# Kernel tuning notes

Hardware: AMD Instinct MI355X
Metric: run time of the kernel (lower is better)

Reference implementation:

```python
import jax, jax.numpy as jnp
import numpy as np

D_MODEL = 1024
D_STATE = 16
EXPAND = 2
D_CONV = 4
D_INNER = EXPAND * D_MODEL          # 2048
DT_RANK = D_MODEL // 16             # 64
B = 2
L = 1024
EPS = 1e-5


def setup_inputs() -> dict:
    key = jax.random.key(0)
    ks = jax.random.split(key, 8)
    s = 0.02
    return {
        "x": jax.random.normal(ks[0], (B, L, D_MODEL), jnp.float32),
        "ln_gamma": jnp.ones((D_MODEL,), jnp.float32),
        "ln_beta": jnp.zeros((D_MODEL,), jnp.float32),
        "in_proj_w": jax.random.normal(ks[1], (2 * D_INNER, D_MODEL), jnp.float32) * s,
        "conv_w": jax.random.normal(ks[2], (D_INNER, 1, D_CONV), jnp.float32) * s,
        "conv_b": jnp.zeros((D_INNER,), jnp.float32),
        "x_proj_w": jax.random.normal(ks[3], (DT_RANK + 2 * D_STATE, D_INNER), jnp.float32) * s,
        "dt_proj_w": jax.random.normal(ks[4], (D_INNER, DT_RANK), jnp.float32) * s,
        "dt_proj_b": jax.random.normal(ks[5], (D_INNER,), jnp.float32) * 0.01,
        "A_log": jnp.log(jnp.tile(jnp.arange(1, D_STATE + 1, dtype=jnp.float32), (D_INNER, 1))),
        "D_skip": jnp.ones((D_INNER,), jnp.float32),
        "out_proj_w": jax.random.normal(ks[6], (D_MODEL, D_INNER), jnp.float32) * s,
    }


def _layernorm(x, g, b):
    mu = jnp.mean(x, axis=-1, keepdims=True)
    var = jnp.mean((x - mu) ** 2, axis=-1, keepdims=True)
    return (x - mu) * jax.lax.rsqrt(var + EPS) * g + b


def _mamba_forward(x, ln_gamma, ln_beta, in_proj_w, conv_w, conv_b,
                   x_proj_w, dt_proj_w, dt_proj_b, A_log, D_skip, out_proj_w):
    residual = x
    xn = _layernorm(x, ln_gamma, ln_beta)

    # in_proj -> split into ssm input u and gate z   (b, l, 2*d_inner)
    xz = jnp.einsum('bld,ed->ble', xn, in_proj_w)
    u, z = jnp.split(xz, 2, axis=-1)

    # causal depthwise conv1d (padding = d_conv-1 on the left, truncated to L)
    uc = jnp.transpose(u, (0, 2, 1))  # (b, d_inner, l)
    uc = jax.lax.conv_general_dilated(
        uc, conv_w, window_strides=(1,), padding=[(D_CONV - 1, 0)],
        feature_group_count=D_INNER,
        dimension_numbers=('NCH', 'OIH', 'NCH'))
    uc = uc + conv_b[None, :, None]
    u = jax.nn.silu(jnp.transpose(uc, (0, 2, 1)))  # (b, l, d_inner)

    # selective SSM
    A = -jnp.exp(A_log)                              # (d_inner, d_state)
    x_dbl = jnp.einsum('bld,ed->ble', u, x_proj_w)   # (b, l, dt_rank+2*n)
    dt, Bm, Cm = jnp.split(x_dbl, [DT_RANK, DT_RANK + D_STATE], axis=-1)
    delta = jax.nn.softplus(jnp.einsum('blr,dr->bld', dt, dt_proj_w) + dt_proj_b)

    def step(h, inputs):
        d_t, B_t, C_t, u_t = inputs            # (b,di) (b,n) (b,n) (b,di)
        dA = jnp.exp(d_t[..., None] * A)       # (b, di, n)
        h = dA * h + (d_t * u_t)[..., None] * B_t[:, None, :]
        y = jnp.einsum('bdn,bn->bd', h, C_t)
        return h, y

    h0 = jnp.zeros((x.shape[0], D_INNER, D_STATE), x.dtype)
    xs = (jnp.moveaxis(delta, 1, 0), jnp.moveaxis(Bm, 1, 0),
          jnp.moveaxis(Cm, 1, 0), jnp.moveaxis(u, 1, 0))
    _, ys = jax.lax.scan(step, h0, xs)
    y = jnp.moveaxis(ys, 0, 1) + u * D_skip     # (b, l, d_inner)

    y = y * jax.nn.silu(z)                      # gated output
    out = jnp.einsum('ble,de->bld', y, out_proj_w)
    # dropout is identity in eval mode
    return out + residual


def reference(x, ln_gamma, ln_beta, in_proj_w, conv_w, conv_b,
              x_proj_w, dt_proj_w, dt_proj_b, A_log, D_skip, out_proj_w):
    return _mamba_forward(x, ln_gamma, ln_beta, in_proj_w, conv_w, conv_b,
                          x_proj_w, dt_proj_w, dt_proj_b, A_log, D_skip, out_proj_w)
```

## Files before the change

### kernel.cpp

```cpp
#include <hip/hip_runtime.h>

#define D_MODEL 1024
#define D_STATE 16
#define D_INNER 2048
#define DT_RANK 64
#define NBATCH 2
#define SEQ_L 1024
#define M_ROWS (NBATCH * SEQ_L)
#define CHUNK 64
#define NCHUNK (SEQ_L / CHUNK)

typedef __bf16 bf16x8 __attribute__((ext_vector_type(8)));
typedef float f32x4 __attribute__((ext_vector_type(4)));
typedef unsigned short u16;
typedef unsigned int u32;

__device__ __forceinline__ float bf2f(u16 h) {
    return __uint_as_float(((unsigned)h) << 16);
}
__device__ __forceinline__ u16 f2bf(float f) {
    unsigned u = __float_as_uint(f);
    u += 0x7fff + ((u >> 16) & 1);
    return (u16)(u >> 16);
}

__global__ __launch_bounds__(256) void cast_all(
    const float* __restrict__ s0, const float* __restrict__ s1,
    const float* __restrict__ s2, const float* __restrict__ s3,
    u16* __restrict__ d0, u16* __restrict__ d1,
    u16* __restrict__ d2, u16* __restrict__ d3) {
    int idx = blockIdx.x * 256 + threadIdx.x;
    if (idx < 4194304) {
        d0[idx] = f2bf(s0[idx]);
    } else if (idx < 6291456) {
        int i = idx - 4194304; d1[i] = f2bf(s1[i]);
    } else if (idx < 6488064) {
        int i = idx - 6291456; d2[i] = f2bf(s2[i]);
    } else {
        int i = idx - 6488064; d3[i] = f2bf(s3[i]);
    }
}

__global__ __launch_bounds__(256) void ln_kernel(
    const float* __restrict__ x, const float* __restrict__ g,
    const float* __restrict__ b, u16* __restrict__ xn) {
    int row = blockIdx.x;
    const float4* xr = (const float4*)(x + (size_t)row * D_MODEL);
    float4 v = xr[threadIdx.x];
    float s  = v.x + v.y + v.z + v.w;
    float ss = v.x * v.x + v.y * v.y + v.z * v.z + v.w * v.w;
#pragma unroll
    for (int off = 32; off > 0; off >>= 1) {
        s  += __shfl_down(s,  off, 64);
        ss += __shfl_down(ss, off, 64);
    }
    __shared__ float sh_s[4], sh_ss[4];
    int wid = threadIdx.x >> 6;
    if ((threadIdx.x & 63) == 0) { sh_s[wid] = s; sh_ss[wid] = ss; }
    __syncthreads();
    float mu  = (sh_s[0] + sh_s[1] + sh_s[2] + sh_s[3]) * (1.0f / D_MODEL);
    float var = (sh_ss[0] + sh_ss[1] + sh_ss[2] + sh_ss[3]) * (1.0f / D_MODEL) - mu * mu;
    float rs = rsqrtf(var + 1e-5f);
    int c0 = threadIdx.x * 4;
    float vv[4] = {v.x, v.y, v.z, v.w};
#pragma unroll
    for (int j = 0; j < 4; j++) {
        int c = c0 + j;
        float o = (vv[j] - mu) * rs * g[c] + b[c];
        xn[(size_t)row * D_MODEL + c] = f2bf(o);
    }
}

template <int BM, int BN, int WM, int WN, int MODE>
__global__ __launch_bounds__(256) void gemm_lds(
    const __bf16* __restrict__ A, const __bf16* __restrict__ W,
    int K, int Ksteps, int ldC,
    float* __restrict__ outF, u16* __restrict__ outB) {
    constexpr int WCOLS = BN / (WN * 16);
    __shared__ __bf16 As[BM * 32];
    __shared__ __bf16 Bs[BN * 32];
    int tid  = threadIdx.x;
    int lane = tid & 63;
    int wid  = tid >> 6;
    int l16  = lane & 15;
    int quad = lane >> 4;
    int wr = wid / WCOLS;
    int wc = wid % WCOLS;
    int m0 = blockIdx.y * BM;
    int n0 = blockIdx.x * BN;
    int kbase = blockIdx.z * Ksteps * 32;

    f32x4 acc[WM][WN];
#pragma unroll
    for (int mi = 0; mi < WM; mi++)
#pragma unroll
        for (int nj = 0; nj < WN; nj++)
            acc[mi][nj] = (f32x4){0.f, 0.f, 0.f, 0.f};

    for (int ki = 0; ki < Ksteps; ki++) {
        int k0 = kbase + ki * 32;
        __syncthreads();
#pragma unroll
        for (int i = 0; i < BM / 64; i++) {
            int t   = i * 256 + tid;
            int row = t >> 2;
            int cg  = (t & 3) ^ ((row >> 1) & 3);
            __builtin_amdgcn_global_load_lds(
                (const __attribute__((address_space(1))) u32*)(A + (size_t)(m0 + row) * K + k0 + cg * 8),
                (__attribute__((address_space(3))) u32*)(As + (i * 256 + wid * 64) * 8),
                16, 0, 0);
        }
#pragma unroll
        for (int i = 0; i < BN / 64; i++) {
            int t   = i * 256 + tid;
            int row = t >> 2;
            int cg  = (t & 3) ^ ((row >> 1) & 3);
            __builtin_amdgcn_global_load_lds(
                (const __attribute__((address_space(1))) u32*)(W + (size_t)(n0 + row) * K + k0 + cg * 8),
                (__attribute__((address_space(3))) u32*)(Bs + (i * 256 + wid * 64) * 8),
                16, 0, 0);
        }
        __syncthreads();

        bf16x8 af[WM], bfr[WN];
#pragma unroll
        for (int mi = 0; mi < WM; mi++) {
            int r  = wr * WM * 16 + mi * 16 + l16;
            int cg = quad ^ ((r >> 1) & 3);
            af[mi] = *(const bf16x8*)(As + r * 32 + cg * 8);
        }
#pragma unroll
        for (int nj = 0; nj < WN; nj++) {
            int r  = wc * WN * 16 + nj * 16 + l16;
            int cg = quad ^ ((r >> 1) & 3);
            bfr[nj] = *(const bf16x8*)(Bs + r * 32 + cg * 8);
        }
#pragma unroll
        for (int mi = 0; mi < WM; mi++)
#pragma unroll
            for (int nj = 0; nj < WN; nj++)
                acc[mi][nj] = __builtin_amdgcn_mfma_f32_16x16x32_bf16(
                    af[mi], bfr[nj], acc[mi][nj], 0, 0, 0);
    }

    float* outP = (MODE == 4) ? outF + (size_t)blockIdx.z * M_ROWS * ldC : outF;
#pragma unroll
    for (int mi = 0; mi < WM; mi++) {
#pragma unroll
        for (int nj = 0; nj < WN; nj++) {
            int col = n0 + wc * WN * 16 + nj * 16 + l16;
#pragma unroll
            for (int r = 0; r < 4; r++) {
                int row = m0 + wr * WM * 16 + mi * 16 + quad * 4 + r;
                float v = acc[mi][nj][r];
                if (MODE == 0) {
                    outB[(size_t)row * ldC + col] = f2bf(v);
                } else {
                    outP[(size_t)row * ldC + col] = v;
                }
            }
        }
    }
}

__global__ __launch_bounds__(256) void out_reduce(
    const float* __restrict__ p, const float* __restrict__ x,
    float* __restrict__ out) {
    int idx = blockIdx.x * 256 + threadIdx.x;
    const int N = M_ROWS * D_MODEL;
    float4 a = ((const float4*)p)[idx];
    float4 b = ((const float4*)(p + N))[idx];
    float4 c = ((const float4*)(p + 2 * N))[idx];
    float4 d = ((const float4*)(p + 3 * N))[idx];
    float4 r = ((const float4*)x)[idx];
    float4 o;
    o.x = a.x + b.x + c.x + d.x + r.x;
    o.y = a.y + b.y + c.y + d.y + r.y;
    o.z = a.z + b.z + c.z + d.z + r.z;
    o.w = a.w + b.w + c.w + d.w + r.w;
    ((float4*)out)[idx] = o;
}

template <int MODE>
__global__ __launch_bounds__(256) void gemm_bt(
    const __bf16* __restrict__ A, const __bf16* __restrict__ W,
    int K, int Ksplit, int Nw, int ldC,
    float* __restrict__ outF, const float* __restrict__ auxF) {
    int lane = threadIdx.x & 63;
    int wid  = threadIdx.x >> 6;
    int m0 = blockIdx.y * 64;
    int n0 = blockIdx.x * 64;
    int kc = blockIdx.z;
    int l16  = lane & 15;
    int quad = lane >> 4;
    int mrow = m0 + wid * 16 + l16;

    const __bf16* ap = A + (size_t)mrow * K + kc * Ksplit + quad * 8;
    const __bf16* wp[4];
#pragma unroll
    for (int j = 0; j < 4; j++) {
        int nc = n0 + j * 16 + l16;
        if (nc > Nw - 1) nc = Nw - 1;
        wp[j] = W + (size_t)nc * K + kc * Ksplit + quad * 8;
    }
    f32x4 acc[4];
#pragma unroll
    for (int j = 0; j < 4; j++) acc[j] = (f32x4){0.f, 0.f, 0.f, 0.f};

    for (int k = 0; k < Ksplit; k += 32) {
        bf16x8 a = *(const bf16x8*)ap;
        ap += 32;
#pragma unroll
        for (int j = 0; j < 4; j++) {
            bf16x8 bfr = *(const bf16x8*)wp[j];
            wp[j] += 32;
            acc[j] = __builtin_amdgcn_mfma_f32_16x16x32_bf16(a, bfr, acc[j], 0, 0, 0);
        }
    }
    float* out = (MODE == 1) ? outF + (size_t)kc * (M_ROWS * 96) : outF;
#pragma unroll
    for (int j = 0; j < 4; j++) {
        int col = n0 + j * 16 + l16;
#pragma unroll
        for (int r = 0; r < 4; r++) {
            int row = m0 + wid * 16 + quad * 4 + r;
            float v = acc[j][r];
            if (MODE == 1) {
                if (col < Nw) out[(size_t)row * ldC + col] = v;
            } else {
                float t = v + auxF[col];
                float sp = (t > 20.f) ? t : log1pf(__expf(t));
                out[(size_t)row * ldC + col] = sp;
            }
        }
    }
}

__global__ __launch_bounds__(256) void xdbl_reduce(
    const float* __restrict__ xdp, float* __restrict__ xd,
    u16* __restrict__ dtb) {
    int idx = blockIdx.x * 256 + threadIdx.x;
    const int N = M_ROWS * 96;
    float v = 0.f;
#pragma unroll
    for (int i = 0; i < 8; i++) v += xdp[idx + i * N];
    xd[idx] = v;
    int mrow = idx / 96;
    int r = idx - mrow * 96;
    if (r < DT_RANK) dtb[mrow * DT_RANK + r] = f2bf(v);
}

__global__ __launch_bounds__(256) void conv_silu(
    const u16* __restrict__ xz, const float* __restrict__ cw,
    const float* __restrict__ cb, u16* __restrict__ uc) {
    int idx = blockIdx.x * 256 + threadIdx.x;
    int d = idx & (D_INNER - 1);
    int m = idx >> 11;
    int t = m & (SEQ_L - 1);
    float s = cb[d];
#pragma unroll
    for (int j = 0; j < 4; j++) {
        int tt = t - 3 + j;
        if (tt >= 0) {
            s += cw[d * 4 + j] *
                 bf2f(xz[(size_t)(m - 3 + j) * (2 * D_INNER) + d]);
        }
    }
    float sig = 1.f / (1.f + __expf(-s));
    uc[idx] = f2bf(s * sig);
}

__global__ __launch_bounds__(256) void scan_chunk(
    const float* __restrict__ delta, const u16* __restrict__ uc,
    const float* __restrict__ xd, const float* __restrict__ A_log,
    float* __restrict__ Pst, float* __restrict__ Sst) {
    __shared__ float Bsh[CHUNK][16];
    int tid  = threadIdx.x;
    int lane = tid & 63;
    int w    = tid >> 6;
    int dsub = lane & 15;
    int g    = lane >> 4;
    int n0   = g * 4;
    int c = blockIdx.x, b = blockIdx.z;
    int d = blockIdx.y * 64 + w * 16 + dsub;
    int mbase = b * SEQ_L + c * CHUNK;

    {
        int row = tid >> 2, q = tid & 3;
        *(float4*)&Bsh[row][q * 4] =
            *(const float4*)(xd + (size_t)(mbase + row) * 96 + DT_RANK + q * 4);
    }
    __syncthreads();

    float a[4];
    {
        float4 a0 = *(const float4*)(A_log + d * D_STATE + n0);
        a[0] = -__expf(a0.x); a[1] = -__expf(a0.y);
        a[2] = -__expf(a0.z); a[3] = -__expf(a0.w);
    }
    float P[4] = {1.f, 1.f, 1.f, 1.f}, S[4] = {0.f, 0.f, 0.f, 0.f};

    for (int t0 = 0; t0 < CHUNK; t0 += 4) {
        float dlv[4], uv[4];
#pragma unroll
        for (int i = 0; i < 4; i++) {
            int m = mbase + t0 + i;
            dlv[i] = delta[(size_t)m * D_INNER + d];
            uv[i]  = bf2f(uc[(size_t)m * D_INNER + d]);
        }
#pragma unroll
        for (int i = 0; i < 4; i++) {
            float c1 = dlv[i] * uv[i];
#pragma unroll
            for (int j = 0; j < 4; j++) {
                float dA = __expf(dlv[i] * a[j]);
                P[j] *= dA;
                S[j] = dA * S[j] + c1 * Bsh[t0 + i][n0 + j];
            }
        }
    }
    size_t s = ((size_t)(b * D_INNER + d) * NCHUNK + c) * D_STATE + n0;
    *(float4*)(Pst + s) = (float4){P[0], P[1], P[2], P[3]};
    *(float4*)(Sst + s) = (float4){S[0], S[1], S[2], S[3]};
}

__global__ __launch_bounds__(256) void scan_combine(
    const float* __restrict__ Pst, const float* __restrict__ Sst,
    float* __restrict__ Hin) {
    int idx = blockIdx.x * 256 + threadIdx.x;
    int bd = idx >> 4;
    int n  = idx & 15;
    float h = 0.f;
#pragma unroll
    for (int c = 0; c < NCHUNK; ++c) {
        size_t s = ((size_t)bd * NCHUNK + c) * D_STATE + n;
        Hin[s] = h;
        h = Pst[s] * h + Sst[s];
    }
}

__global__ __launch_bounds__(256) void scan_apply(
    const float* __restrict__ delta, const u16* __restrict__ uc,
    const float* __restrict__ xd, const u16* __restrict__ xz,
    const float* __restrict__ A_log, const float* __restrict__ Dsk,
    const float* __restrict__ Hin, u16* __restrict__ yg) {
    __shared__ float BCs[CHUNK][32];
    int tid  = threadIdx.x;
    int lane = tid & 63;
    int w    = tid >> 6;
    int dsub = lane & 15;
    int g    = lane >> 4;
    int n0   = g * 4;
    int c = blockIdx.x, b = blockIdx.z;
    int d = blockIdx.y * 64 + w * 16 + dsub;
    int mbase = b * SEQ_L + c * CHUNK;

    {
#pragma unroll
        for (int i = 0; i < 2; i++) {
            int idx = i * 256 + tid;
            int row = idx >> 3, q = idx & 7;
            *(float4*)&BCs[row][q * 4] =
                *(const float4*)(xd + (size_t)(mbase + row) * 96 + DT_RANK + q * 4);
        }
    }
    __syncthreads();

    float a[4];
    {
        float4 a0 = *(const float4*)(A_log + d * D_STATE + n0);
        a[0] = -__expf(a0.x); a[1] = -__expf(a0.y);
        a[2] = -__expf(a0.z); a[3] = -__expf(a0.w);
    }
    float h[4];
    {
        float4 h0 = *(const float4*)(Hin +
            (((size_t)(b * D_INNER + d) * NCHUNK + c) * D_STATE + n0));
        h[0] = h0.x; h[1] = h0.y; h[2] = h0.z; h[3] = h0.w;
    }
    float dsk = Dsk[d];

    for (int t0 = 0; t0 < CHUNK; t0 += 4) {
        float dlv[4], uv[4], zv[4];
#pragma unroll
        for (int i = 0; i < 4; i++) {
            int m = mbase + t0 + i;
            dlv[i] = delta[(size_t)m * D_INNER + d];
            uv[i]  = bf2f(uc[(size_t)m * D_INNER + d]);
            zv[i]  = bf2f(xz[(size_t)m * (2 * D_INNER) + D_INNER + d]);
        }
#pragma unroll
        for (int i = 0; i < 4; i++) {
            int t = t0 + i;
            float c1 = dlv[i] * uv[i];
            float y = 0.f;
#pragma unroll
            for (int j = 0; j < 4; j++) {
                float dA = __expf(dlv[i] * a[j]);
                h[j] = dA * h[j] + c1 * BCs[t][n0 + j];
                y += h[j] * BCs[t][16 + n0 + j];
            }
            y += __shfl_xor(y, 16);
            y += __shfl_xor(y, 32);
            if (g == 0) {
                float z = zv[i];
                float yv = y + uv[i] * dsk;
                float gt = z / (1.f + __expf(-z));
                yg[(size_t)(mbase + t) * D_INNER + d] = f2bf(yv * gt);
            }
        }
    }
}

extern "C" void kernel_launch(void* const* d_in, const int* in_sizes, int n_in,
                              void* d_out, int out_size, void* d_ws, size_t ws_size,
                              hipStream_t stream) {
    const float* x         = (const float*)d_in[0];
    const float* ln_g      = (const float*)d_in[1];
    const float* ln_b      = (const float*)d_in[2];
    const float* in_proj_w = (const float*)d_in[3];
    const float* conv_w    = (const float*)d_in[4];
    const float* conv_b    = (const float*)d_in[5];
    const float* x_proj_w  = (const float*)d_in[6];
    const float* dt_proj_w = (const float*)d_in[7];
    const float* dt_proj_b = (const float*)d_in[8];
    const float* A_log     = (const float*)d_in[9];
    const float* Dsk       = (const float*)d_in[10];
    const float* out_proj_w= (const float*)d_in[11];

    char* ws = (char*)d_ws;
    u16* xn   = (u16*)ws;    ws += (size_t)M_ROWS * D_MODEL * 2;
    u16* xz   = (u16*)ws;    ws += (size_t)M_ROWS * 2 * D_INNER * 2;
    u16* ucv  = (u16*)ws;    ws += (size_t)M_ROWS * D_INNER * 2;
    float* xd = (float*)ws;  ws += (size_t)M_ROWS * 96 * 4;
    u16* dtb  = (u16*)ws;    ws += (size_t)M_ROWS * DT_RANK * 2;
    float* dl = (float*)ws;  ws += (size_t)M_ROWS * D_INNER * 4;
    u16* yg   = (u16*)ws;    ws += (size_t)M_ROWS * D_INNER * 2;
    u16* w_in = (u16*)ws;    ws += (size_t)4194304 * 2;
    u16* w_out= (u16*)ws;    ws += (size_t)2097152 * 2;
    u16* w_xp = (u16*)ws;    ws += (size_t)196608 * 2;
    u16* w_dt = (u16*)ws;

    float* Pst = (float*)w_in;
    float* Sst = (float*)w_in + 1048576;
    float* Hin = (float*)xn;
    float* xdp = (float*)yg;
    float* opart = (float*)xz;

    cast_all<<<25856, 256, 0, stream>>>(in_proj_w, out_proj_w, x_proj_w, dt_proj_w,
                                        w_in, w_out, w_xp, w_dt);
    ln_kernel<<<M_ROWS, 256, 0, stream>>>(x, ln_g, ln_b, xn);
    gemm_lds<64, 128, 4, 2, 0><<<dim3(4096 / 128, M_ROWS / 64, 1), 256, 0, stream>>>(
        (const __bf16*)xn, (const __bf16*)w_in, D_MODEL, D_MODEL / 32, 2 * D_INNER,
        nullptr, xz);
    conv_silu<<<(M_ROWS * D_INNER) / 256, 256, 0, stream>>>(xz, conv_w, conv_b, ucv);
    gemm_bt<1><<<dim3(2, 32, 8), 256, 0, stream>>>(
        (const __bf16*)ucv, (const __bf16*)w_xp, D_INNER, D_INNER / 8, 96, 96,
        xdp, nullptr);
    xdbl_reduce<<<(M_ROWS * 96) / 256, 256, 0, stream>>>(xdp, xd, dtb);
    gemm_bt<2><<<dim3(32, 32, 1), 256, 0, stream>>>(
        (const __bf16*)dtb, (const __bf16*)w_dt, DT_RANK, DT_RANK, D_INNER,
        D_INNER, dl, dt_proj_b);
    dim3 sgrid(NCHUNK, D_INNER / 64, NBATCH);
    scan_chunk<<<sgrid, 256, 0, stream>>>(dl, ucv, xd, A_log, Pst, Sst);
    scan_combine<<<(NBATCH * D_INNER * D_STATE) / 256, 256, 0, stream>>>(Pst, Sst, Hin);
    scan_apply<<<sgrid, 256, 0, stream>>>(dl, ucv, xd, xz, A_log, Dsk, Hin, yg);
    gemm_lds<64, 128, 4, 2, 4><<<dim3(1024 / 128, M_ROWS / 64, 4), 256, 0, stream>>>(
        (const __bf16*)yg, (const __bf16*)w_out, D_INNER, D_INNER / 4 / 32, D_MODEL,
        opart, nullptr);
    out_reduce<<<(M_ROWS * D_MODEL / 4) / 256, 256, 0, stream>>>(
        opart, x, (float*)d_out);
}
```

Baseline: 273.9 us.

## Fuse dt_proj GEMM and softplus into scan kernels, merge cast with layernorm

Drops the standalone dt_proj GEMM that wrote a full fp32 delta tensor (M x 2048) to global memory. Each scan_chunk and scan_apply block now recomputes its own 64x64 delta tile with MFMA from the bf16 dt low-rank input and keeps it in shared memory. The weight cast and layernorm are also merged into a single launch to save one kernel launch. The cost is that delta is computed twice (once per scan pass), and the extra shared memory and MFMA prologue may reduce occupancy in the scan kernels.

```diff
diff --git a/kernel.cpp b/kernel.cpp
--- a/kernel.cpp
+++ b/kernel.cpp
@@ -24,27 +24,28 @@
     return (u16)(u >> 16);
 }
 
-__global__ __launch_bounds__(256) void cast_all(
+__global__ __launch_bounds__(256) void prep(
     const float* __restrict__ s0, const float* __restrict__ s1,
     const float* __restrict__ s2, const float* __restrict__ s3,
     u16* __restrict__ d0, u16* __restrict__ d1,
-    u16* __restrict__ d2, u16* __restrict__ d3) {
-    int idx = blockIdx.x * 256 + threadIdx.x;
-    if (idx < 4194304) {
-        d0[idx] = f2bf(s0[idx]);
-    } else if (idx < 6291456) {
-        int i = idx - 4194304; d1[i] = f2bf(s1[i]);
-    } else if (idx < 6488064) {
-        int i = idx - 6291456; d2[i] = f2bf(s2[i]);
-    } else {
-        int i = idx - 6488064; d3[i] = f2bf(s3[i]);
-    }
-}
-
-__global__ __launch_bounds__(256) void ln_kernel(
+    u16* __restrict__ d2, u16* __restrict__ d3,
     const float* __restrict__ x, const float* __restrict__ g,
     const float* __restrict__ b, u16* __restrict__ xn) {
-    int row = blockIdx.x;
+    int blk = blockIdx.x;
+    if (blk < 25856) {
+        int idx = blk * 256 + threadIdx.x;
+        if (idx < 4194304) {
+            d0[idx] = f2bf(s0[idx]);
+        } else if (idx < 6291456) {
+            int i = idx - 4194304; d1[i] = f2bf(s1[i]);
+        } else if (idx < 6488064) {
+            int i = idx - 6291456; d2[i] = f2bf(s2[i]);
+        } else {
+            int i = idx - 6488064; d3[i] = f2bf(s3[i]);
+        }
+        return;
+    }
+    int row = blk - 25856;
     const float4* xr = (const float4*)(x + (size_t)row * D_MODEL);
     float4 v = xr[threadIdx.x];
     float s  = v.x + v.y + v.z + v.w;
@@ -181,11 +182,9 @@
     ((float4*)out)[idx] = o;
 }
 
-template <int MODE>
-__global__ __launch_bounds__(256) void gemm_bt(
+__global__ __launch_bounds__(256) void gemm_xproj(
     const __bf16* __restrict__ A, const __bf16* __restrict__ W,
-    int K, int Ksplit, int Nw, int ldC,
-    float* __restrict__ outF, const float* __restrict__ auxF) {
+    int K, int Ksplit, int Nw, int ldC, float* __restrict__ outF) {
     int lane = threadIdx.x & 63;
     int wid  = threadIdx.x >> 6;
     int m0 = blockIdx.y * 64;
@@ -217,21 +216,14 @@
             acc[j] = __builtin_amdgcn_mfma_f32_16x16x32_bf16(a, bfr, acc[j], 0, 0, 0);
         }
     }
-    float* out = (MODE == 1) ? outF + (size_t)kc * (M_ROWS * 96) : outF;
+    float* out = outF + (size_t)kc * (M_ROWS * 96);
 #pragma unroll
     for (int j = 0; j < 4; j++) {
         int col = n0 + j * 16 + l16;
 #pragma unroll
         for (int r = 0; r < 4; r++) {
             int row = m0 + wid * 16 + quad * 4 + r;
-            float v = acc[j][r];
-            if (MODE == 1) {
-                if (col < Nw) out[(size_t)row * ldC + col] = v;
-            } else {
-                float t = v + auxF[col];
-                float sp = (t > 20.f) ? t : log1pf(__expf(t));
-                out[(size_t)row * ldC + col] = sp;
-            }
+            if (col < Nw) out[(size_t)row * ldC + col] = acc[j][r];
         }
     }
 }
@@ -270,10 +262,44 @@
     uc[idx] = f2bf(s * sig);
 }
 
+
+__device__ __forceinline__ void delta_tile(
+    const __bf16* __restrict__ dtb, const __bf16* __restrict__ wdt,
+    const float* __restrict__ dtbias, int mbase, int d0,
+    int w, int l16, int quad, float (*dlS)[64]) {
+    f32x4 acc[4];
+#pragma unroll
+    for (int j = 0; j < 4; j++) acc[j] = (f32x4){0.f, 0.f, 0.f, 0.f};
+    const __bf16* ap = dtb + (size_t)(mbase + w * 16 + l16) * DT_RANK + quad * 8;
+#pragma unroll
+    for (int kk = 0; kk < 2; kk++) {
+        bf16x8 av = *(const bf16x8*)(ap + kk * 32);
+#pragma unroll
+        for (int j = 0; j < 4; j++) {
+            bf16x8 bv = *(const bf16x8*)(wdt +
+                (size_t)(d0 + j * 16 + l16) * DT_RANK + kk * 32 + quad * 8);
+            acc[j] = __builtin_amdgcn_mfma_f32_16x16x32_bf16(av, bv, acc[j], 0, 0, 0);
+        }
+    }
+#pragma unroll
+    for (int j = 0; j < 4; j++) {
+        int dcol = j * 16 + l16;
+        float bias = dtbias[d0 + dcol];
+#pragma unroll
+        for (int r = 0; r < 4; r++) {
+            float tv = acc[j][r] + bias;
+            dlS[w * 16 + quad * 4 + r][dcol] = (tv > 20.f) ? tv : log1pf(__expf(tv));
+        }
+    }
+}
+
 __global__ __launch_bounds__(256) void scan_chunk(
-    const float* __restrict__ delta, const u16* __restrict__ uc,
-    const float* __restrict__ xd, const float* __restrict__ A_log,
+    const __bf16* __restrict__ dtb, const __bf16* __restrict__ wdt,
+    const float* __restrict__ dtbias,
+    const u16* __restrict__ uc, const float* __restrict__ xd,
+    const float* __restrict__ A_log,
     float* __restrict__ Pst, float* __restrict__ Sst) {
+    __shared__ float dlS[CHUNK][64];
     __shared__ float Bsh[CHUNK][16];
     int tid  = threadIdx.x;
     int lane = tid & 63;
@@ -282,9 +308,12 @@
     int g    = lane >> 4;
     int n0   = g * 4;
     int c = blockIdx.x, b = blockIdx.z;
-    int d = blockIdx.y * 64 + w * 16 + dsub;
+    int d0 = blockIdx.y * 64;
+    int dloc = w * 16 + dsub;
+    int d = d0 + dloc;
     int mbase = b * SEQ_L + c * CHUNK;
 
+    delta_tile(dtb, wdt, dtbias, mbase, d0, w, dsub, g, dlS);
     {
         int row = tid >> 2, q = tid & 3;
         *(float4*)&Bsh[row][q * 4] =
@@ -305,8 +334,8 @@
 #pragma unroll
         for (int i = 0; i < 4; i++) {
             int m = mbase + t0 + i;
-            dlv[i] = delta[(size_t)m * D_INNER + d];
             uv[i]  = bf2f(uc[(size_t)m * D_INNER + d]);
+            dlv[i] = dlS[t0 + i][dloc];
         }
 #pragma unroll
         for (int i = 0; i < 4; i++) {
@@ -340,10 +369,13 @@
 }
 
 __global__ __launch_bounds__(256) void scan_apply(
-    const float* __restrict__ delta, const u16* __restrict__ uc,
-    const float* __restrict__ xd, const u16* __restrict__ xz,
-    const float* __restrict__ A_log, const float* __restrict__ Dsk,
-    const float* __restrict__ Hin, u16* __restrict__ yg) {
+    const __bf16* __restrict__ dtb, const __bf16* __restrict__ wdt,
+    const float* __restrict__ dtbias,
+    const u16* __restrict__ uc, const float* __restrict__ xd,
+    const u16* __restrict__ xz, const float* __restrict__ A_log,
+    const float* __restrict__ Dsk, const float* __restrict__ Hin,
+    u16* __restrict__ yg) {
+    __shared__ float dlS[CHUNK][64];
     __shared__ float BCs[CHUNK][32];
     int tid  = threadIdx.x;
     int lane = tid & 63;
@@ -352,9 +384,12 @@
     int g    = lane >> 4;
     int n0   = g * 4;
     int c = blockIdx.x, b = blockIdx.z;
-    int d = blockIdx.y * 64 + w * 16 + dsub;
+    int d0 = blockIdx.y * 64;
+    int dloc = w * 16 + dsub;
+    int d = d0 + dloc;
     int mbase = b * SEQ_L + c * CHUNK;
 
+    delta_tile(dtb, wdt, dtbias, mbase, d0, w, dsub, g, dlS);
     {
 #pragma unroll
         for (int i = 0; i < 2; i++) {
@@ -385,9 +420,9 @@
 #pragma unroll
         for (int i = 0; i < 4; i++) {
             int m = mbase + t0 + i;
-            dlv[i] = delta[(size_t)m * D_INNER + d];
             uv[i]  = bf2f(uc[(size_t)m * D_INNER + d]);
             zv[i]  = bf2f(xz[(size_t)m * (2 * D_INNER) + D_INNER + d]);
+            dlv[i] = dlS[t0 + i][dloc];
         }
 #pragma unroll
         for (int i = 0; i < 4; i++) {
@@ -434,7 +469,7 @@
     u16* ucv  = (u16*)ws;    ws += (size_t)M_ROWS * D_INNER * 2;
     float* xd = (float*)ws;  ws += (size_t)M_ROWS * 96 * 4;
     u16* dtb  = (u16*)ws;    ws += (size_t)M_ROWS * DT_RANK * 2;
-    float* dl = (float*)ws;  ws += (size_t)M_ROWS * D_INNER * 4;
+    ws += (size_t)M_ROWS * D_INNER * 4;
     u16* yg   = (u16*)ws;    ws += (size_t)M_ROWS * D_INNER * 2;
     u16* w_in = (u16*)ws;    ws += (size_t)4194304 * 2;
     u16* w_out= (u16*)ws;    ws += (size_t)2097152 * 2;
@@ -447,24 +482,23 @@
     float* xdp = (float*)yg;
     float* opart = (float*)xz;
 
-    cast_all<<<25856, 256, 0, stream>>>(in_proj_w, out_proj_w, x_proj_w, dt_proj_w,
-                                        w_in, w_out, w_xp, w_dt);
-    ln_kernel<<<M_ROWS, 256, 0, stream>>>(x, ln_g, ln_b, xn);
+    prep<<<25856 + M_ROWS, 256, 0, stream>>>(
+        in_proj_w, out_proj_w, x_proj_w, dt_proj_w, w_in, w_out, w_xp, w_dt,
+        x, ln_g, ln_b, xn);
     gemm_lds<64, 128, 4, 2, 0><<<dim3(4096 / 128, M_ROWS / 64, 1), 256, 0, stream>>>(
         (const __bf16*)xn, (const __bf16*)w_in, D_MODEL, D_MODEL / 32, 2 * D_INNER,
         nullptr, xz);
     conv_silu<<<(M_ROWS * D_INNER) / 256, 256, 0, stream>>>(xz, conv_w, conv_b, ucv);
-    gemm_bt<1><<<dim3(2, 32, 8), 256, 0, stream>>>(
-        (const __bf16*)ucv, (const __bf16*)w_xp, D_INNER, D_INNER / 8, 96, 96,
-        xdp, nullptr);
+    gemm_xproj<<<dim3(2, 32, 8), 256, 0, stream>>>(
+        (const __bf16*)ucv, (const __bf16*)w_xp, D_INNER, D_INNER / 8, 96, 96, xdp);
     xdbl_reduce<<<(M_ROWS * 96) / 256, 256, 0, stream>>>(xdp, xd, dtb);
-    gemm_bt<2><<<dim3(32, 32, 1), 256, 0, stream>>>(
-        (const __bf16*)dtb, (const __bf16*)w_dt, DT_RANK, DT_RANK, D_INNER,
-        D_INNER, dl, dt_proj_b);
     dim3 sgrid(NCHUNK, D_INNER / 64, NBATCH);
-    scan_chunk<<<sgrid, 256, 0, stream>>>(dl, ucv, xd, A_log, Pst, Sst);
+    scan_chunk<<<sgrid, 256, 0, stream>>>(
+        (const __bf16*)dtb, (const __bf16*)w_dt, dt_proj_b, ucv, xd, A_log, Pst, Sst);
     scan_combine<<<(NBATCH * D_INNER * D_STATE) / 256, 256, 0, stream>>>(Pst, Sst, Hin);
-    scan_apply<<<sgrid, 256, 0, stream>>>(dl, ucv, xd, xz, A_log, Dsk, Hin, yg);
+    scan_apply<<<sgrid, 256, 0, stream>>>(
+        (const __bf16*)dtb, (const __bf16*)w_dt, dt_proj_b, ucv, xd, xz,
+        A_log, Dsk, Hin, yg);
     gemm_lds<64, 128, 4, 2, 4><<<dim3(1024 / 128, M_ROWS / 64, 4), 256, 0, stream>>>(
         (const __bf16*)yg, (const __bf16*)w_out, D_INNER, D_INNER / 4 / 32, D_MODEL,
         opart, nullptr);
```

Result: slower. 284.6 us (+3.9%).
